# Kernel tuning notes

Measured on AMD Instinct MI355X. Metric: run time of the kernel, lower is better.

The kernel has to match this reference:

```python
import jax, jax.numpy as jnp
import numpy as np

H, C, L = 2, 32, 25
EPS = 1e-5


def setup_inputs() -> dict:
    key = jax.random.key(0)
    ks = jax.random.split(key, 12)
    N, E = 20000, 100000
    x_input = jax.random.normal(ks[0], (N, 5), jnp.float32)
    # edges with no self loops (module uses add_self_loops=True, which first removes them)
    src = jax.random.randint(ks[1], (L, E), 0, N, dtype=jnp.int32)
    off = jax.random.randint(ks[2], (L, E), 1, N, dtype=jnp.int32)
    dst = (src + off) % N
    edge_indices = jnp.stack([src, dst], axis=1)              # [L, 2, E]
    edge_weights = jax.random.uniform(ks[3], (L, E, 1), jnp.float32)
    g = lambda k, shp, fan: jax.random.normal(k, shp, jnp.float32) / np.float32(np.sqrt(fan))
    return {
        "x_input": x_input,
        "edge_indices": edge_indices,
        "edge_weights": edge_weights,
        "Wl": g(ks[4], (L, 5, H * C), 5),
        "bl": jnp.zeros((L, H * C), jnp.float32),
        "Wr": g(ks[5], (L, 5, H * C), 5),
        "br": jnp.zeros((L, H * C), jnp.float32),
        "We": g(ks[6], (L, 1, H * C), 1),
        "att": g(ks[7], (L, H, C), C),
        "conv_bias": jnp.zeros((L, C), jnp.float32),
        "gamma1": jnp.ones((L, C), jnp.float32),
        "beta1": jnp.zeros((L, C), jnp.float32),
        "W1": g(ks[8], (800, 800), 800),
        "b1": jnp.zeros((800,), jnp.float32),
        "W2": g(ks[9], (800, 5), 800),
        "b2": jnp.zeros((5,), jnp.float32),
    }


def reference(x_input, edge_indices, edge_weights, Wl, bl, Wr, br, We, att,
              conv_bias, gamma1, beta1, W1, b1, W2, b2):
    N = x_input.shape[0]
    loops = jnp.arange(N, dtype=edge_indices.dtype)

    def layer(carry, p):
        ei, ew, wl, bl_, wr, br_, we, a, cb, g_, be_ = p
        src, dst = ei[0], ei[1]
        ones_e = jnp.ones((src.shape[0],), x_input.dtype)
        # add_self_loops with fill_value='mean': loop attr = mean of incoming edge attrs
        cnt = jax.ops.segment_sum(ones_e, dst, num_segments=N)
        loop_attr = jax.ops.segment_sum(ew, dst, num_segments=N) / jnp.maximum(cnt, 1.0)[:, None]
        s2 = jnp.concatenate([src, loops])
        d2 = jnp.concatenate([dst, loops])
        ea = jnp.concatenate([ew, loop_attr], axis=0)          # [E+N, 1]
        xl = (x_input @ wl + bl_).reshape(N, H, C)             # source transform
        xr = (x_input @ wr + br_).reshape(N, H, C)             # target transform
        eh = jax.nn.leaky_relu(xl[s2] + xr[d2] + (ea @ we).reshape(-1, H, C), 0.2)
        alpha = jnp.einsum('ehc,hc->eh', eh, a)                # [E+N, H]
        amax = jax.ops.segment_max(alpha, d2, num_segments=N)
        alpha = jnp.exp(alpha - amax[d2])
        alpha = alpha / jax.ops.segment_sum(alpha, d2, num_segments=N)[d2]
        msg = (xl[s2] * alpha[:, :, None]).reshape(-1, H * C)
        deg = jax.ops.segment_sum(jnp.ones((s2.shape[0],), x_input.dtype), d2, num_segments=N)
        out = (jax.ops.segment_sum(msg, d2, num_segments=N) / deg[:, None]).reshape(N, H, C)
        out = out.mean(axis=1) + cb                            # concat=False -> mean over heads, + bias
        mu = out.mean(axis=0)
        var = out.var(axis=0)                                  # BatchNorm1d, training-mode batch stats
        out = g_ * (out - mu) * jax.lax.rsqrt(var + EPS) + be_
        return carry, jax.nn.leaky_relu(out, 0.01)

    _, hs = jax.lax.scan(layer, None,
                         (edge_indices, edge_weights, Wl, bl, Wr, br, We, att,
                          conv_bias, gamma1, beta1))            # [L, N, C]
    h = jnp.transpose(hs, (1, 0, 2)).reshape(N, L * C)          # cat along feature dim
    h = jax.nn.relu(h @ W1 + b1)
    return h @ W2 + b2
```

## Files before the change

### kernel.cpp

```cpp
#include <hip/hip_runtime.h>
#include <hip/hip_bf16.h>

#define N_NODES 20000
#define N_EDGES 100000
#define N_LAYERS 25
#define NPAD 20096
#define EPS_BN 1e-5f
#define LOG2E 1.44269504088896340736f
#define NL_NN (N_LAYERS * N_NODES)
#define TOTAL_E (N_LAYERS * N_EDGES)
#define SCAN_BLKS ((NL_NN + 1023) / 1024)
#define QUARTER_N 5000
#define CNT_BLKS (N_LAYERS * 4)
#define W1T_END (CNT_BLKS + 700)
#define XPAD_END (W1T_END + 157)
#define HPAD_BLKS 75
#define PREP_BLKS (XPAD_END + HPAD_BLKS)
#define EDGE_BLKS ((TOTAL_E + 1023) / 1024)
#define FILL_BLKS (EDGE_BLKS + SCAN_BLKS)
#define NGRP 14
#define NPW 8
#define NPL (N_NODES / NPW)
#define ATTN_WAVES (NL_NN / NPW)
#define ATTN_BLKS (ATTN_WAVES / 4)

typedef short short8 __attribute__((ext_vector_type(8)));
typedef short short4v __attribute__((ext_vector_type(4)));
typedef float floatx4 __attribute__((ext_vector_type(4)));
typedef float float8v __attribute__((ext_vector_type(8)));
typedef int int8v __attribute__((ext_vector_type(8)));
typedef int int2v __attribute__((ext_vector_type(2)));

template <int PAT>
__device__ __forceinline__ float swz(float v) {
  return __int_as_float(__builtin_amdgcn_ds_swizzle(__float_as_int(v), PAT));
}

template <int CTRL>
__device__ __forceinline__ float dpp_add(float v) {
  int r = __builtin_amdgcn_update_dpp(0, __float_as_int(v), CTRL, 0xF, 0xF, true);
  return v + __int_as_float(r);
}

__device__ __forceinline__ float ldbf(const unsigned short* __restrict__ p, int idx) {
  return __uint_as_float((unsigned)p[idx] << 16);
}

__device__ __forceinline__ unsigned short bfbits(float v) {
  return __builtin_bit_cast(unsigned short, (__hip_bfloat16)v);
}

__device__ __forceinline__ void gl_lds16(const short* g, short* l) {
  __builtin_amdgcn_global_load_lds(
      (const __attribute__((address_space(1))) void*)g,
      (__attribute__((address_space(3))) void*)l, 16, 0, 0);
}

__device__ __forceinline__ int8v sload8(const void* p) {
  int8v r;
  asm volatile(
      "s_load_dwordx8 %0, %1, 0x0\n\t"
      "s_waitcnt lgkmcnt(0)"
      : "=s"(r)
      : "s"(p));
  return r;
}

__device__ __forceinline__ void sload_rp(const void* p, int8v& a, int8v& b) {
  asm volatile(
      "s_load_dwordx8 %0, %2, 0x0\n\t"
      "s_load_dwordx8 %1, %2, 0x20\n\t"
      "s_waitcnt lgkmcnt(0)"
      : "=s"(a), "=s"(b)
      : "s"(p));
}

__device__ __forceinline__ void sload_chunk(const void* p, int8v& r0, int8v& r1,
                                            int8v& r2, int8v& r3) {
  asm volatile(
      "s_load_dwordx8 %0, %4, 0x0\n\t"
      "s_load_dwordx8 %1, %4, 0x20\n\t"
      "s_load_dwordx8 %2, %4, 0x40\n\t"
      "s_load_dwordx8 %3, %4, 0x60\n\t"
      "s_waitcnt lgkmcnt(0)"
      : "=s"(r0), "=s"(r1), "=s"(r2), "=s"(r3)
      : "s"(p));
}

__device__ __forceinline__ void red4(float& p0, float& p1, float& p2, float& p3) {
  asm volatile(
      "s_nop 1\n\t"
      "v_add_f32_dpp %0, %0, %0 quad_perm:[1,0,3,2] row_mask:0xf bank_mask:0xf\n\t"
      "v_add_f32_dpp %1, %1, %1 quad_perm:[1,0,3,2] row_mask:0xf bank_mask:0xf\n\t"
      "v_add_f32_dpp %2, %2, %2 quad_perm:[1,0,3,2] row_mask:0xf bank_mask:0xf\n\t"
      "v_add_f32_dpp %3, %3, %3 quad_perm:[1,0,3,2] row_mask:0xf bank_mask:0xf\n\t"
      "v_add_f32_dpp %0, %0, %0 quad_perm:[2,3,0,1] row_mask:0xf bank_mask:0xf\n\t"
      "v_add_f32_dpp %1, %1, %1 quad_perm:[2,3,0,1] row_mask:0xf bank_mask:0xf\n\t"
      "v_add_f32_dpp %2, %2, %2 quad_perm:[2,3,0,1] row_mask:0xf bank_mask:0xf\n\t"
      "v_add_f32_dpp %3, %3, %3 quad_perm:[2,3,0,1] row_mask:0xf bank_mask:0xf\n\t"
      "v_add_f32_dpp %0, %0, %0 row_half_mirror row_mask:0xf bank_mask:0xf\n\t"
      "v_add_f32_dpp %1, %1, %1 row_half_mirror row_mask:0xf bank_mask:0xf\n\t"
      "v_add_f32_dpp %2, %2, %2 row_half_mirror row_mask:0xf bank_mask:0xf\n\t"
      "v_add_f32_dpp %3, %3, %3 row_half_mirror row_mask:0xf bank_mask:0xf\n\t"
      "v_add_f32_dpp %0, %0, %0 row_mirror row_mask:0xf bank_mask:0xf\n\t"
      "v_add_f32_dpp %1, %1, %1 row_mirror row_mask:0xf bank_mask:0xf\n\t"
      "v_add_f32_dpp %2, %2, %2 row_mirror row_mask:0xf bank_mask:0xf\n\t"
      "v_add_f32_dpp %3, %3, %3 row_mirror row_mask:0xf bank_mask:0xf\n\t"
      "s_nop 1"
      : "+v"(p0), "+v"(p1), "+v"(p2), "+v"(p3));
}

__device__ __forceinline__ float red1(float p) {
  asm volatile(
      "s_nop 1\n\t"
      "v_add_f32_dpp %0, %0, %0 quad_perm:[1,0,3,2] row_mask:0xf bank_mask:0xf\n\t"
      "s_nop 1\n\t"
      "v_add_f32_dpp %0, %0, %0 quad_perm:[2,3,0,1] row_mask:0xf bank_mask:0xf\n\t"
      "s_nop 1\n\t"
      "v_add_f32_dpp %0, %0, %0 row_half_mirror row_mask:0xf bank_mask:0xf\n\t"
      "s_nop 1\n\t"
      "v_add_f32_dpp %0, %0, %0 row_mirror row_mask:0xf bank_mask:0xf\n\t"
      "s_nop 1"
      : "+v"(p));
  return p;
}

__global__ __launch_bounds__(1024) void prep_kernel(
    const int* __restrict__ ei, const float* __restrict__ x,
    const float* __restrict__ W1, int* __restrict__ cnt,
    int* __restrict__ rank, float* __restrict__ xpad,
    __hip_bfloat16* __restrict__ W1bT, unsigned short* __restrict__ hn) {
  __shared__ int smem[QUARTER_N];
  int b = blockIdx.x;
  if (b < CNT_BLKS) {
    int l = b >> 2, base = (b & 3) * QUARTER_N;
    for (int i = threadIdx.x; i < QUARTER_N; i += 1024) smem[i] = 0;
    __syncthreads();
    const int* dstp = ei + (size_t)l * 2 * N_EDGES + N_EDGES;
    int* rkp = rank + l * N_EDGES;
    for (int e = threadIdx.x; e < N_EDGES; e += 1024) {
      int d = dstp[e] - base;
      if ((unsigned)d < (unsigned)QUARTER_N) rkp[e] = atomicAdd(&smem[d], 1);
    }
    __syncthreads();
    int* outp = cnt + l * N_NODES + base;
    for (int i = threadIdx.x; i < QUARTER_N; i += 1024) outp[i] = smem[i];
  } else if (b < W1T_END) {
    float* tile = (float*)smem;
    int bb = b - CNT_BLKS;
    int j0 = (bb % 28) * 32, k0 = (bb / 28) * 32;
    int tx = threadIdx.x & 31, ty = threadIdx.x >> 5;
    tile[ty * 33 + tx] = (j0 + tx < 800) ? W1[(k0 + ty) * 800 + j0 + tx] : 0.f;
    __syncthreads();
    W1bT[(size_t)(j0 + ty) * 800 + k0 + tx] = (__hip_bfloat16)tile[tx * 33 + ty];
  } else if (b < XPAD_END) {
    int idx = (b - W1T_END) * 1024 + threadIdx.x;
    if (idx < N_NODES * 8) {
      int nn = idx >> 3, k = idx & 7;
      xpad[idx] = (k < 5) ? x[nn * 5 + k] : 0.f;
    }
  } else {
    int idx = (b - XPAD_END) * 1024 + threadIdx.x;
    const int per_l = (NPAD - N_NODES) * 32;
    if (idx < N_LAYERS * per_l) {
      int l = idx / per_l;
      int rem = idx - l * per_l;
      hn[((size_t)l * NPAD + N_NODES) * 32 + rem] = 0;
    }
  }
}

__global__ __launch_bounds__(1024) void scan_a(const int* __restrict__ cnt,
                                               int* __restrict__ scn,
                                               int* __restrict__ btot,
                                               float* __restrict__ gsum,
                                               float* __restrict__ gsumsq) {
  int t = threadIdx.x, b = blockIdx.x;
  int i = b * 1024 + t;
  int lane = t & 63, wv = t >> 6;
  int v = (i < NL_NN) ? cnt[i] : 0;
  int sc = v;
#pragma unroll
  for (int off = 1; off < 64; off <<= 1) {
    int u = __shfl_up(sc, off);
    if (lane >= off) sc += u;
  }
  __shared__ int ws[16];
  if (lane == 63) ws[wv] = sc;
  __syncthreads();
  if (t < 16) {
    int xx = ws[t];
#pragma unroll
    for (int off = 1; off < 16; off <<= 1) {
      int u = __shfl_up(xx, off);
      if (t >= off) xx += u;
    }
    ws[t] = xx;
  }
  __syncthreads();
  int bofs = wv ? ws[wv - 1] : 0;
  if (i < NL_NN) scn[i] = bofs + sc - v;
  if (t == 0) btot[b] = ws[15];
  if (b == 200 && t < N_LAYERS * 32) {
    gsum[t] = 0.f;
    gsumsq[t] = 0.f;
  }
}

__global__ __launch_bounds__(512) void scan_b(const int* __restrict__ btot,
                                              int* __restrict__ boff) {
  int t = threadIdx.x;
  int lane = t & 63, wv = t >> 6;
  int v = (t < SCAN_BLKS) ? btot[t] : 0;
  int sc = v;
#pragma unroll
  for (int off = 1; off < 64; off <<= 1) {
    int u = __shfl_up(sc, off);
    if (lane >= off) sc += u;
  }
  __shared__ int ws[8];
  if (lane == 63) ws[wv] = sc;
  __syncthreads();
  if (t < 8) {
    int xx = ws[t];
#pragma unroll
    for (int off = 1; off < 8; off <<= 1) {
      int u = __shfl_up(xx, off);
      if (t >= off) xx += u;
    }
    ws[t] = xx;
  }
  __syncthreads();
  int bofs = wv ? ws[wv - 1] : 0;
  if (t < SCAN_BLKS) boff[t] = bofs + sc - v;
}

__global__ __launch_bounds__(1024) void fill_kernel(const int* __restrict__ ei,
                                                    const float* __restrict__ ew,
                                                    const int* __restrict__ scn,
                                                    const int* __restrict__ boff,
                                                    const int* __restrict__ rank,
                                                    const float* __restrict__ xpad,
                                                    int* __restrict__ rowptr,
                                                    float* __restrict__ epf) {
  int b = blockIdx.x;
  if (b < EDGE_BLKS) {
    int idx = b * 1024 + threadIdx.x;
    if (idx >= TOTAL_E) return;
    int l = idx / N_EDGES, e = idx - l * N_EDGES;
    int src = ei[(size_t)l * 2 * N_EDGES + e];
    int dst = ei[(size_t)l * 2 * N_EDGES + N_EDGES + e];
    int g = l * N_NODES + dst;
    int pos = scn[g] + boff[g >> 10] + rank[idx];
    float w = ew[(size_t)l * N_EDGES + e];
    float4 xv = *(const float4*)(xpad + (size_t)src * 8);
    float x4v = xpad[(size_t)src * 8 + 4];
    float8v r;
    r[0] = w; r[1] = xv.x; r[2] = xv.y; r[3] = xv.z; r[4] = xv.w; r[5] = x4v;
    r[6] = 0.f; r[7] = 0.f;
    *(float8v*)(epf + (size_t)pos * 8) = r;
  } else {
    int i = (b - EDGE_BLKS) * 1024 + threadIdx.x;
    if (i < NL_NN) rowptr[i] = scn[i] + boff[i >> 10];
    if (i < 31) rowptr[NL_NN + i] = TOTAL_E;
    if (i < 4) {
      float8v z = {0.f, 0.f, 0.f, 0.f, 0.f, 0.f, 0.f, 0.f};
      *(float8v*)(epf + (size_t)(TOTAL_E + i) * 8) = z;
    }
  }
}

__global__ __launch_bounds__(256) void attn_kernel(
    const float* __restrict__ xpad, const int* __restrict__ rowptr,
    const float* __restrict__ epf,
    const float* __restrict__ Wl, const float* __restrict__ bl,
    const float* __restrict__ Wr, const float* __restrict__ br,
    const float* __restrict__ We, const float* __restrict__ att,
    const float* __restrict__ cbias, unsigned short* __restrict__ out_pre) {
  int b = blockIdx.x;
  const int q = ATTN_BLKS >> 3, r = ATTN_BLKS & 7;
  int xcd = b & 7, ib = b >> 3;
  int nb = (xcd < r ? xcd * (q + 1) : r * (q + 1) + (xcd - r) * q) + ib;
  int wid = __builtin_amdgcn_readfirstlane(nb * 4 + (threadIdx.x >> 6));
  int lane = threadIdx.x & 63;
  int l = wid / NPL;
  int n0 = (wid - l * NPL) * NPW;

  float wlv0 = Wl[(l * 5 + 0) * 64 + lane];
  float wlv1 = Wl[(l * 5 + 1) * 64 + lane];
  float wlv2 = Wl[(l * 5 + 2) * 64 + lane];
  float wlv3 = Wl[(l * 5 + 3) * 64 + lane];
  float wlv4 = Wl[(l * 5 + 4) * 64 + lane];
  float wr0 = Wr[(l * 5 + 0) * 64 + lane];
  float wr1 = Wr[(l * 5 + 1) * 64 + lane];
  float wr2 = Wr[(l * 5 + 2) * 64 + lane];
  float wr3 = Wr[(l * 5 + 3) * 64 + lane];
  float wr4 = Wr[(l * 5 + 4) * 64 + lane];
  float blv = bl[l * 64 + lane];
  float brv = br[l * 64 + lane];
  float wev = We[l * 64 + lane];
  float att2v = att[l * 64 + lane] * LOG2E;
  float cbv = cbias[l * 32 + (lane & 31)];

  int8v rpa, rpb;
  sload_rp(rowptr + (size_t)wid * 8, rpa, rpb);

#pragma unroll
  for (int i = 0; i < NPW; i++) {
    int st = rpa[i & 7];
    int en = (i == 7) ? rpb[0] : rpa[(i + 1) & 7];
    int cnt = en - st;

    int8v xn = sload8(xpad + (size_t)(n0 + i) * 8);
    float x0 = __int_as_float(xn[0]), x1 = __int_as_float(xn[1]);
    float x2 = __int_as_float(xn[2]), x3 = __int_as_float(xn[3]);
    float x4 = __int_as_float(xn[4]);
    float xrn = brv, xln = blv;
    xrn = fmaf(x0, wr0, xrn); xrn = fmaf(x1, wr1, xrn);
    xrn = fmaf(x2, wr2, xrn); xrn = fmaf(x3, wr3, xrn);
    xrn = fmaf(x4, wr4, xrn);
    xln = fmaf(x0, wlv0, xln); xln = fmaf(x1, wlv1, xln);
    xln = fmaf(x2, wlv2, xln); xln = fmaf(x3, wlv3, xln);
    xln = fmaf(x4, wlv4, xln);

    float ssum = 0.f, acc = 0.f, ewsum = 0.f;
    int nchunk = (cnt + 3) >> 2;
    const float* pch = epf + (size_t)st * 8;
    for (int c = 0; c < nchunk; c++) {
      int8v r0, r1, r2, r3;
      sload_chunk(pch, r0, r1, r2, r3);
      pch += 32;
      int m = cnt - c * 4;
      float xa[4], pk[4], wv[4];
#pragma unroll
      for (int k = 0; k < 4; k++) {
        int8v rr = (k == 0) ? r0 : (k == 1) ? r1 : (k == 2) ? r2 : r3;
        bool ok = k < m;
        int wbits = ok ? rr[0] : 0;
        wv[k] = __int_as_float(wbits);
        float a = fmaf(__int_as_float(rr[1]), wlv0, blv);
        a = fmaf(__int_as_float(rr[2]), wlv1, a);
        a = fmaf(__int_as_float(rr[3]), wlv2, a);
        a = fmaf(__int_as_float(rr[4]), wlv3, a);
        a = fmaf(__int_as_float(rr[5]), wlv4, a);
        xa[k] = a;
        float bias = __int_as_float(ok ? 0 : (int)0xff800000);
        float v = a + fmaf(wv[k], wev, xrn);
        float lk = fmaxf(v, 0.2f * v);
        pk[k] = fmaf(lk, att2v, bias);
      }
      red4(pk[0], pk[1], pk[2], pk[3]);
#pragma unroll
      for (int k = 0; k < 4; k++) pk[k] += swz<0x401F>(pk[k]);
#pragma unroll
      for (int k = 0; k < 4; k++) {
        float pe = __builtin_amdgcn_exp2f(pk[k]);
        ssum += pe;
        acc = fmaf(xa[k], pe, acc);
        ewsum += wv[k];
      }
    }
    {
      float w = ewsum * __builtin_amdgcn_rcpf(fmaxf((float)cnt, 1.f));
      float v = xln + fmaf(w, wev, xrn);
      float lk = fmaxf(v, 0.2f * v);
      float p = red1(lk * att2v);
      p += swz<0x401F>(p);
      float pe = __builtin_amdgcn_exp2f(p);
      ssum += pe;
      acc = fmaf(xln, pe, acc);
    }
    float outv = acc * __builtin_amdgcn_rcpf(ssum * (float)(cnt + 1));
    float o2 = outv + __shfl_xor(outv, 32);
    if (lane < 32)
      out_pre[((size_t)wid * NPW + i) * 32 + lane] = bfbits(0.5f * o2 + cbv);
  }
}

__global__ __launch_bounds__(256) void stats_kernel(const unsigned short* __restrict__ out_pre,
                                                    float* __restrict__ gsum,
                                                    float* __restrict__ gsumsq) {
  int l = blockIdx.x >> 4, chunk = blockIdx.x & 15;
  int t = threadIdx.x;
  int c = t & 31, nsub = t >> 5;
  int n0 = chunk * 1250;
  float s1 = 0.f, s2 = 0.f;
  for (int n = n0 + nsub; n < n0 + 1250; n += 8) {
    float v = ldbf(out_pre, (l * N_NODES + n) * 32 + c);
    s1 += v; s2 += v * v;
  }
  __shared__ float l1[256], l2[256];
  l1[t] = s1; l2[t] = s2;
  __syncthreads();
  for (int off = 128; off >= 32; off >>= 1) {
    if (t < off) { l1[t] += l1[t + off]; l2[t] += l2[t + off]; }
    __syncthreads();
  }
  if (t < 32) {
    atomicAdd(&gsum[l * 32 + t], l1[t]);
    atomicAdd(&gsumsq[l * 32 + t], l2[t]);
  }
}

__global__ __launch_bounds__(256) void norm_kernel(const unsigned short* __restrict__ out_pre,
                                                   const float* __restrict__ gsum,
                                                   const float* __restrict__ gsumsq,
                                                   const float* __restrict__ gamma,
                                                   const float* __restrict__ beta,
                                                   unsigned short* __restrict__ hn) {
  int idx = blockIdx.x * 256 + threadIdx.x;
  int l = idx / (N_NODES * 8);
  int rem = idx - l * (N_NODES * 8);
  int n = rem >> 3, q = rem & 7;
  int c0 = q * 4;
  short4v v4 = *(const short4v*)(out_pre + (l * N_NODES + n) * 32 + c0);
  short4v o;
#pragma unroll
  for (int i = 0; i < 4; i++) {
    int c = c0 + i;
    float mu = gsum[l * 32 + c] * (1.f / N_NODES);
    float var = gsumsq[l * 32 + c] * (1.f / N_NODES) - mu * mu;
    float vv = __uint_as_float((unsigned)(unsigned short)v4[i] << 16);
    float v = gamma[l * 32 + c] * (vv - mu) * rsqrtf(var + EPS_BN) + beta[l * 32 + c];
    v = v > 0.f ? v : 0.01f * v;
    o[i] = (short)bfbits(v);
  }
  *(short4v*)(hn + ((size_t)l * NPAD + n) * 32 + c0) = o;
}

__global__ __launch_bounds__(256) void gemm1_kernel(const short* __restrict__ hn,
                                                    const short* __restrict__ W1bT,
                                                    const float* __restrict__ b1,
                                                    const float* __restrict__ W2,
                                                    float* __restrict__ p) {
  __shared__ __align__(16) short As[128 * 32];
  __shared__ __align__(16) short Bs[128 * 32];
  int t = threadIdx.x;
  int n0 = blockIdx.x * 128, m0 = blockIdx.y * 128;
  int wave = t >> 6, lane = t & 63;
  int wr = wave >> 1, wc = wave & 1;
  int mrow = lane & 15, quad = lane >> 4;
  floatx4 acc[4][4];
#pragma unroll
  for (int i = 0; i < 4; i++)
#pragma unroll
    for (int j = 0; j < 4; j++) acc[i][j] = (floatx4){0.f, 0.f, 0.f, 0.f};

  int r0 = t >> 2, s0 = t & 3;
  int r1 = (t + 256) >> 2, s1 = (t + 256) & 3;
  const short* aG0 = hn + (m0 + r0) * 32 + s0 * 8;
  const short* aG1 = hn + (m0 + r1) * 32 + s1 * 8;
  const short* bG0 = W1bT + (n0 + r0) * 800 + s0 * 8;
  const short* bG1 = W1bT + (n0 + r1) * 800 + s1 * 8;
  const int ak = NPAD * 32;
  short* aD0 = As + wave * 512;
  short* aD1 = As + 2048 + wave * 512;
  short* bD0 = Bs + wave * 512;
  short* bD1 = Bs + 2048 + wave * 512;

  for (int kt = 0; kt < 25; kt++) {
    gl_lds16(aG0, aD0);
    gl_lds16(aG1, aD1);
    gl_lds16(bG0, bD0);
    gl_lds16(bG1, bD1);
    aG0 += ak; aG1 += ak; bG0 += 32; bG1 += 32;
    __syncthreads();
    short8 af[4], bfr[4];
#pragma unroll
    for (int i = 0; i < 4; i++)
      af[i] = *(const short8*)(&As[(wr * 64 + i * 16 + mrow) * 32 + quad * 8]);
#pragma unroll
    for (int j = 0; j < 4; j++)
      bfr[j] = *(const short8*)(&Bs[(wc * 64 + j * 16 + mrow) * 32 + quad * 8]);
#pragma unroll
    for (int i = 0; i < 4; i++)
#pragma unroll
      for (int j = 0; j < 4; j++)
        acc[i][j] = __builtin_amdgcn_mfma_f32_16x16x32_bf16(af[i], bfr[j], acc[i][j], 0, 0, 0);
    __syncthreads();
  }

  float w2v[4][5];
  float b1v[4];
#pragma unroll
  for (int j = 0; j < 4; j++) {
    int col = n0 + wc * 64 + j * 16 + mrow;
    bool ok = col < 800;
    b1v[j] = ok ? b1[col] : 0.f;
#pragma unroll
    for (int jj = 0; jj < 5; jj++) w2v[j][jj] = ok ? W2[col * 5 + jj] : 0.f;
  }
  int grp = blockIdx.x * 2 + wc;
#pragma unroll
  for (int i = 0; i < 4; i++) {
#pragma unroll
    for (int r = 0; r < 4; r++) {
      float s[5] = {0.f, 0.f, 0.f, 0.f, 0.f};
#pragma unroll
      for (int j = 0; j < 4; j++) {
        float v = fmaxf(acc[i][j][r] + b1v[j], 0.f);
#pragma unroll
        for (int jj = 0; jj < 5; jj++) s[jj] = fmaf(v, w2v[j][jj], s[jj]);
      }
#pragma unroll
      for (int jj = 0; jj < 5; jj++) {
        s[jj] = dpp_add<0xB1>(s[jj]);
        s[jj] = dpp_add<0x4E>(s[jj]);
        s[jj] = dpp_add<0x141>(s[jj]);
        s[jj] = dpp_add<0x140>(s[jj]);
      }
      int row = m0 + wr * 64 + i * 16 + quad * 4 + r;
      if (mrow == 0) {
#pragma unroll
        for (int jj = 0; jj < 5; jj++)
          p[(row * NGRP + grp) * 5 + jj] = s[jj];
      }
    }
  }
}

__global__ __launch_bounds__(256) void gemm2r_kernel(const float* __restrict__ p,
                                                     const float* __restrict__ b2,
                                                     float* __restrict__ out) {
  int idx = blockIdx.x * 256 + threadIdx.x;
  if (idx >= N_NODES * 5) return;
  int row = idx / 5, jj = idx - row * 5;
  float s = b2[jj];
#pragma unroll
  for (int g = 0; g < NGRP; g++) s += p[(row * NGRP + g) * 5 + jj];
  out[idx] = s;
}

extern "C" void kernel_launch(void* const* d_in, const int* in_sizes, int n_in,
                              void* d_out, int out_size, void* d_ws, size_t ws_size,
                              hipStream_t stream) {
  const float* x    = (const float*)d_in[0];
  const int*   ei   = (const int*)d_in[1];
  const float* ew   = (const float*)d_in[2];
  const float* Wl   = (const float*)d_in[3];
  const float* bl   = (const float*)d_in[4];
  const float* Wr   = (const float*)d_in[5];
  const float* br   = (const float*)d_in[6];
  const float* We   = (const float*)d_in[7];
  const float* att  = (const float*)d_in[8];
  const float* cb   = (const float*)d_in[9];
  const float* gam  = (const float*)d_in[10];
  const float* bet  = (const float*)d_in[11];
  const float* W1   = (const float*)d_in[12];
  const float* b1   = (const float*)d_in[13];
  const float* W2   = (const float*)d_in[14];
  const float* b2   = (const float*)d_in[15];

  char* ws = (char*)d_ws;
  size_t off = 0;
  auto alloc = [&](size_t bytes) {
    void* p = ws + off;
    off = (off + bytes + 255) & ~(size_t)255;
    return p;
  };
  int* cnt     = (int*)alloc((size_t)NL_NN * 4);
  int* scn     = (int*)alloc((size_t)NL_NN * 4);
  int* btot    = (int*)alloc(SCAN_BLKS * 4);
  int* boff    = (int*)alloc(SCAN_BLKS * 4);
  int* rank    = (int*)alloc((size_t)TOTAL_E * 4);
  int* rowptr  = (int*)alloc((size_t)(NL_NN + 32) * 4);
  float* epf   = (float*)alloc((size_t)TOTAL_E * 32 + 128);
  unsigned short* out_pre = (unsigned short*)alloc((size_t)NL_NN * 32 * 2);
  float* gsum   = (float*)alloc(N_LAYERS * 32 * 4);
  float* gsumsq = (float*)alloc(N_LAYERS * 32 * 4);
  float* xpad   = (float*)alloc((size_t)N_NODES * 8 * 4);
  __hip_bfloat16* w1t = (__hip_bfloat16*)alloc((size_t)896 * 800 * 2);
  float* pbuf = (float*)alloc((size_t)NPAD * NGRP * 5 * 4);
  unsigned short* hn = (unsigned short*)alloc((size_t)N_LAYERS * NPAD * 32 * 2);

  prep_kernel<<<PREP_BLKS, 1024, 0, stream>>>(ei, x, W1, cnt, rank, xpad, w1t, hn);
  scan_a<<<SCAN_BLKS, 1024, 0, stream>>>(cnt, scn, btot, gsum, gsumsq);
  scan_b<<<1, 512, 0, stream>>>(btot, boff);
  fill_kernel<<<FILL_BLKS, 1024, 0, stream>>>(ei, ew, scn, boff, rank, xpad,
                                              rowptr, epf);
  attn_kernel<<<ATTN_BLKS, 256, 0, stream>>>(
      xpad, rowptr, epf, Wl, bl, Wr, br, We, att, cb, out_pre);
  stats_kernel<<<N_LAYERS * 16, 256, 0, stream>>>(out_pre, gsum, gsumsq);
  norm_kernel<<<(NL_NN * 8) / 256, 256, 0, stream>>>(
      out_pre, gsum, gsumsq, gam, bet, hn);
  gemm1_kernel<<<dim3(7, 157), 256, 0, stream>>>(
      (const short*)hn, (const short*)w1t, b1, W2, pbuf);
  gemm2r_kernel<<<(N_NODES * 5 + 255) / 256, 256, 0, stream>>>(
      pbuf, b2, (float*)d_out);
}
```

Before: 496.7 us.

## Stage block's edge records into LDS via direct global-to-LDS loads in attn kernel

Each attention block now cooperatively copies the contiguous range of packed edge records for its 32 nodes into a 16 KB shared buffer using global-to-LDS loads. The per-node edge loop then reads from LDS instead of issuing scalar loads to global memory, falling back to global loads when a block's edges exceed the 512-record capacity. The aim is to replace serialized scalar-memory latency with one bulk prefetch. In exchange it adds a block-wide barrier, LDS use that may lower occupancy, and a larger padded edge buffer so the copy can overrun safely.

```diff
diff --git a/kernel.cpp b/kernel.cpp
--- a/kernel.cpp
+++ b/kernel.cpp
@@ -23,6 +23,7 @@
 #define NPL (N_NODES / NPW)
 #define ATTN_WAVES (NL_NN / NPW)
 #define ATTN_BLKS (ATTN_WAVES / 4)
+#define CAP_E 512
 
 typedef short short8 __attribute__((ext_vector_type(8)));
 typedef short short4v __attribute__((ext_vector_type(4)));
@@ -277,12 +278,28 @@
     const float* __restrict__ Wr, const float* __restrict__ br,
     const float* __restrict__ We, const float* __restrict__ att,
     const float* __restrict__ cbias, unsigned short* __restrict__ out_pre) {
+  __shared__ __align__(16) float ldse[CAP_E * 8];
   int b = blockIdx.x;
   const int q = ATTN_BLKS >> 3, r = ATTN_BLKS & 7;
   int xcd = b & 7, ib = b >> 3;
   int nb = (xcd < r ? xcd * (q + 1) : r * (q + 1) + (xcd - r) * q) + ib;
-  int wid = __builtin_amdgcn_readfirstlane(nb * 4 + (threadIdx.x >> 6));
-  int lane = threadIdx.x & 63;
+  int tid = threadIdx.x;
+  int w = tid >> 6, lane = tid & 63;
+  int wid0 = nb * 4;
+  int wid = __builtin_amdgcn_readfirstlane(wid0 + w);
+
+  int bs = __builtin_amdgcn_readfirstlane(rowptr[wid0 * 8]);
+  int be = __builtin_amdgcn_readfirstlane(rowptr[wid0 * 8 + 32]);
+  int want = be - bs + 4;
+  int staged = want < CAP_E ? want : CAP_E;
+  int rounds = (staged * 32 + 4095) >> 12;
+  const char* srcb = (const char*)epf + (size_t)bs * 32;
+  for (int rr2 = 0; rr2 < rounds; rr2++) {
+    int blk16 = (rr2 * 4 + w) * 64;
+    gl_lds16((const short*)(srcb + (size_t)(blk16 + lane) * 16),
+             (short*)((char*)ldse + (size_t)blk16 * 16));
+  }
+
   int l = wid / NPL;
   int n0 = (wid - l * NPL) * NPW;
 
@@ -305,6 +322,8 @@
   int8v rpa, rpb;
   sload_rp(rowptr + (size_t)wid * 8, rpa, rpb);
 
+  __syncthreads();
+
 #pragma unroll
   for (int i = 0; i < NPW; i++) {
     int st = rpa[i & 7];
@@ -325,24 +344,41 @@
 
     float ssum = 0.f, acc = 0.f, ewsum = 0.f;
     int nchunk = (cnt + 3) >> 2;
-    const float* pch = epf + (size_t)st * 8;
     for (int c = 0; c < nchunk; c++) {
-      int8v r0, r1, r2, r3;
-      sload_chunk(pch, r0, r1, r2, r3);
-      pch += 32;
       int m = cnt - c * 4;
+      int g = st + c * 4;
+      float aw[4], av[4][5];
+      if (g - bs + 4 <= staged) {
+        int co = (g - bs) * 32;
+#pragma unroll
+        for (int k = 0; k < 4; k++) {
+          float4 p0 = *(const float4*)((const char*)ldse + (co + k * 32));
+          float4 p1 = *(const float4*)((const char*)ldse + (co + k * 32 + 16));
+          aw[k] = p0.x;
+          av[k][0] = p0.y; av[k][1] = p0.z; av[k][2] = p0.w;
+          av[k][3] = p1.x; av[k][4] = p1.y;
+        }
+      } else {
+        int8v r0, r1, r2, r3;
+        sload_chunk(epf + (size_t)g * 8, r0, r1, r2, r3);
+#pragma unroll
+        for (int k = 0; k < 4; k++) {
+          int8v rrv = (k == 0) ? r0 : (k == 1) ? r1 : (k == 2) ? r2 : r3;
+          aw[k] = __int_as_float(rrv[0]);
+#pragma unroll
+          for (int j = 0; j < 5; j++) av[k][j] = __int_as_float(rrv[1 + j]);
+        }
+      }
       float xa[4], pk[4], wv[4];
 #pragma unroll
       for (int k = 0; k < 4; k++) {
-        int8v rr = (k == 0) ? r0 : (k == 1) ? r1 : (k == 2) ? r2 : r3;
         bool ok = k < m;
-        int wbits = ok ? rr[0] : 0;
-        wv[k] = __int_as_float(wbits);
-        float a = fmaf(__int_as_float(rr[1]), wlv0, blv);
-        a = fmaf(__int_as_float(rr[2]), wlv1, a);
-        a = fmaf(__int_as_float(rr[3]), wlv2, a);
-        a = fmaf(__int_as_float(rr[4]), wlv3, a);
-        a = fmaf(__int_as_float(rr[5]), wlv4, a);
+        wv[k] = ok ? aw[k] : 0.f;
+        float a = fmaf(av[k][0], wlv0, blv);
+        a = fmaf(av[k][1], wlv1, a);
+        a = fmaf(av[k][2], wlv2, a);
+        a = fmaf(av[k][3], wlv3, a);
+        a = fmaf(av[k][4], wlv4, a);
         xa[k] = a;
         float bias = __int_as_float(ok ? 0 : (int)0xff800000);
         float v = a + fmaf(wv[k], wev, xrn);
@@ -361,8 +397,8 @@
       }
     }
     {
-      float w = ewsum * __builtin_amdgcn_rcpf(fmaxf((float)cnt, 1.f));
-      float v = xln + fmaf(w, wev, xrn);
+      float wsl = ewsum * __builtin_amdgcn_rcpf(fmaxf((float)cnt, 1.f));
+      float v = xln + fmaf(wsl, wev, xrn);
       float lk = fmaxf(v, 0.2f * v);
       float p = red1(lk * att2v);
       p += swz<0x401F>(p);
@@ -564,7 +600,7 @@
   int* boff    = (int*)alloc(SCAN_BLKS * 4);
   int* rank    = (int*)alloc((size_t)TOTAL_E * 4);
   int* rowptr  = (int*)alloc((size_t)(NL_NN + 32) * 4);
-  float* epf   = (float*)alloc((size_t)TOTAL_E * 32 + 128);
+  float* epf   = (float*)alloc((size_t)TOTAL_E * 32 + 32768);
   unsigned short* out_pre = (unsigned short*)alloc((size_t)NL_NN * 32 * 2);
   float* gsum   = (float*)alloc(N_LAYERS * 32 * 4);
   float* gsumsq = (float*)alloc(N_LAYERS * 32 * 4);
```

Result: no change. 492.9 us (-0.8%).

## Materialize self-loop slots in CSR and fuse final reduction via atomics

Applied to the files above, without the earlier changes.

The per-destination edge-weight sum is now accumulated during counting, and each node's self-loop (mean weight plus its features) is written as an extra CSR slot. This lets the attention kernel handle the loop in the same chunked loop instead of a separate cross-lane reduction tail. The gemm2 reduction kernel and its partial buffer are removed. The norm kernel initializes the output with b2, and gemm1 atomically adds its partial row sums into the output. This trades one launch and a tail path for extra CSR storage and float atomics whose summation order is nondeterministic.

```diff
diff --git a/kernel.cpp b/kernel.cpp
--- a/kernel.cpp
+++ b/kernel.cpp
@@ -9,6 +9,7 @@
 #define LOG2E 1.44269504088896340736f
 #define NL_NN (N_LAYERS * N_NODES)
 #define TOTAL_E (N_LAYERS * N_EDGES)
+#define TOTAL_SLOTS (TOTAL_E + NL_NN)
 #define SCAN_BLKS ((NL_NN + 1023) / 1024)
 #define QUARTER_N 5000
 #define CNT_BLKS (N_LAYERS * 4)
@@ -18,7 +19,6 @@
 #define PREP_BLKS (XPAD_END + HPAD_BLKS)
 #define EDGE_BLKS ((TOTAL_E + 1023) / 1024)
 #define FILL_BLKS (EDGE_BLKS + SCAN_BLKS)
-#define NGRP 14
 #define NPW 8
 #define NPL (N_NODES / NPW)
 #define ATTN_WAVES (NL_NN / NPW)
@@ -110,41 +110,39 @@
       : "+v"(p0), "+v"(p1), "+v"(p2), "+v"(p3));
 }
 
-__device__ __forceinline__ float red1(float p) {
-  asm volatile(
-      "s_nop 1\n\t"
-      "v_add_f32_dpp %0, %0, %0 quad_perm:[1,0,3,2] row_mask:0xf bank_mask:0xf\n\t"
-      "s_nop 1\n\t"
-      "v_add_f32_dpp %0, %0, %0 quad_perm:[2,3,0,1] row_mask:0xf bank_mask:0xf\n\t"
-      "s_nop 1\n\t"
-      "v_add_f32_dpp %0, %0, %0 row_half_mirror row_mask:0xf bank_mask:0xf\n\t"
-      "s_nop 1\n\t"
-      "v_add_f32_dpp %0, %0, %0 row_mirror row_mask:0xf bank_mask:0xf\n\t"
-      "s_nop 1"
-      : "+v"(p));
-  return p;
-}
-
 __global__ __launch_bounds__(1024) void prep_kernel(
-    const int* __restrict__ ei, const float* __restrict__ x,
-    const float* __restrict__ W1, int* __restrict__ cnt,
-    int* __restrict__ rank, float* __restrict__ xpad,
+    const int* __restrict__ ei, const float* __restrict__ ew,
+    const float* __restrict__ x, const float* __restrict__ W1,
+    int* __restrict__ cnt, int* __restrict__ rank,
+    float* __restrict__ wsumg, float* __restrict__ xpad,
     __hip_bfloat16* __restrict__ W1bT, unsigned short* __restrict__ hn) {
   __shared__ int smem[QUARTER_N];
+  __shared__ float fsm[QUARTER_N];
   int b = blockIdx.x;
   if (b < CNT_BLKS) {
     int l = b >> 2, base = (b & 3) * QUARTER_N;
-    for (int i = threadIdx.x; i < QUARTER_N; i += 1024) smem[i] = 0;
+    for (int i = threadIdx.x; i < QUARTER_N; i += 1024) {
+      smem[i] = 0;
+      fsm[i] = 0.f;
+    }
     __syncthreads();
     const int* dstp = ei + (size_t)l * 2 * N_EDGES + N_EDGES;
+    const float* ewp = ew + (size_t)l * N_EDGES;
     int* rkp = rank + l * N_EDGES;
     for (int e = threadIdx.x; e < N_EDGES; e += 1024) {
       int d = dstp[e] - base;
-      if ((unsigned)d < (unsigned)QUARTER_N) rkp[e] = atomicAdd(&smem[d], 1);
+      if ((unsigned)d < (unsigned)QUARTER_N) {
+        rkp[e] = atomicAdd(&smem[d], 1);
+        atomicAdd(&fsm[d], ewp[e]);
+      }
     }
     __syncthreads();
     int* outp = cnt + l * N_NODES + base;
-    for (int i = threadIdx.x; i < QUARTER_N; i += 1024) outp[i] = smem[i];
+    float* wp = wsumg + l * N_NODES + base;
+    for (int i = threadIdx.x; i < QUARTER_N; i += 1024) {
+      outp[i] = smem[i];
+      wp[i] = fsm[i];
+    }
   } else if (b < W1T_END) {
     float* tile = (float*)smem;
     int bb = b - CNT_BLKS;
@@ -178,7 +176,7 @@
   int t = threadIdx.x, b = blockIdx.x;
   int i = b * 1024 + t;
   int lane = t & 63, wv = t >> 6;
-  int v = (i < NL_NN) ? cnt[i] : 0;
+  int v = (i < NL_NN) ? cnt[i] + 1 : 0;
   int sc = v;
 #pragma unroll
   for (int off = 1; off < 64; off <<= 1) {
@@ -240,6 +238,7 @@
                                                     const int* __restrict__ scn,
                                                     const int* __restrict__ boff,
                                                     const int* __restrict__ rank,
+                                                    const float* __restrict__ wsumg,
                                                     const float* __restrict__ xpad,
                                                     int* __restrict__ rowptr,
                                                     float* __restrict__ epf) {
@@ -261,11 +260,24 @@
     *(float8v*)(epf + (size_t)pos * 8) = r;
   } else {
     int i = (b - EDGE_BLKS) * 1024 + threadIdx.x;
-    if (i < NL_NN) rowptr[i] = scn[i] + boff[i >> 10];
-    if (i < 31) rowptr[NL_NN + i] = TOTAL_E;
+    if (i < NL_NN) {
+      int st = scn[i] + boff[i >> 10];
+      int en = (i + 1 < NL_NN) ? scn[i + 1] + boff[(i + 1) >> 10] : TOTAL_SLOTS;
+      rowptr[i] = st;
+      int cw = en - st - 1;
+      float wm = wsumg[i] * __builtin_amdgcn_rcpf(fmaxf((float)cw, 1.f));
+      int n = i - (i / N_NODES) * N_NODES;
+      float4 xv = *(const float4*)(xpad + (size_t)n * 8);
+      float x4v = xpad[(size_t)n * 8 + 4];
+      float8v r;
+      r[0] = wm; r[1] = xv.x; r[2] = xv.y; r[3] = xv.z; r[4] = xv.w; r[5] = x4v;
+      r[6] = 0.f; r[7] = 0.f;
+      *(float8v*)(epf + (size_t)(en - 1) * 8) = r;
+    }
+    if (i < 31) rowptr[NL_NN + i] = TOTAL_SLOTS;
     if (i < 4) {
       float8v z = {0.f, 0.f, 0.f, 0.f, 0.f, 0.f, 0.f, 0.f};
-      *(float8v*)(epf + (size_t)(TOTAL_E + i) * 8) = z;
+      *(float8v*)(epf + (size_t)(TOTAL_SLOTS + i) * 8) = z;
     }
   }
 }
@@ -309,45 +321,35 @@
   for (int i = 0; i < NPW; i++) {
     int st = rpa[i & 7];
     int en = (i == 7) ? rpb[0] : rpa[(i + 1) & 7];
-    int cnt = en - st;
+    int valid = en - st;
 
     int8v xn = sload8(xpad + (size_t)(n0 + i) * 8);
-    float x0 = __int_as_float(xn[0]), x1 = __int_as_float(xn[1]);
-    float x2 = __int_as_float(xn[2]), x3 = __int_as_float(xn[3]);
-    float x4 = __int_as_float(xn[4]);
-    float xrn = brv, xln = blv;
-    xrn = fmaf(x0, wr0, xrn); xrn = fmaf(x1, wr1, xrn);
-    xrn = fmaf(x2, wr2, xrn); xrn = fmaf(x3, wr3, xrn);
-    xrn = fmaf(x4, wr4, xrn);
-    xln = fmaf(x0, wlv0, xln); xln = fmaf(x1, wlv1, xln);
-    xln = fmaf(x2, wlv2, xln); xln = fmaf(x3, wlv3, xln);
-    xln = fmaf(x4, wlv4, xln);
-
-    float ssum = 0.f, acc = 0.f, ewsum = 0.f;
-    int nchunk = (cnt + 3) >> 2;
-    const float* pch = epf + (size_t)st * 8;
+    float xrn = brv;
+    xrn = fmaf(__int_as_float(xn[0]), wr0, xrn);
+    xrn = fmaf(__int_as_float(xn[1]), wr1, xrn);
+    xrn = fmaf(__int_as_float(xn[2]), wr2, xrn);
+    xrn = fmaf(__int_as_float(xn[3]), wr3, xrn);
+    xrn = fmaf(__int_as_float(xn[4]), wr4, xrn);
+
+    float ssum = 0.f, acc = 0.f;
+    int nchunk = (valid + 3) >> 2;
     for (int c = 0; c < nchunk; c++) {
       int8v r0, r1, r2, r3;
-      sload_chunk(pch, r0, r1, r2, r3);
-      pch += 32;
-      int m = cnt - c * 4;
-      float xa[4], pk[4], wv[4];
+      sload_chunk(epf + (size_t)(st + c * 4) * 8, r0, r1, r2, r3);
+      int m = valid - c * 4;
+      float xa[4], pk[4];
 #pragma unroll
       for (int k = 0; k < 4; k++) {
         int8v rr = (k == 0) ? r0 : (k == 1) ? r1 : (k == 2) ? r2 : r3;
-        bool ok = k < m;
-        int wbits = ok ? rr[0] : 0;
-        wv[k] = __int_as_float(wbits);
         float a = fmaf(__int_as_float(rr[1]), wlv0, blv);
         a = fmaf(__int_as_float(rr[2]), wlv1, a);
         a = fmaf(__int_as_float(rr[3]), wlv2, a);
         a = fmaf(__int_as_float(rr[4]), wlv3, a);
         a = fmaf(__int_as_float(rr[5]), wlv4, a);
         xa[k] = a;
-        float bias = __int_as_float(ok ? 0 : (int)0xff800000);
-        float v = a + fmaf(wv[k], wev, xrn);
+        float v = a + fmaf(__int_as_float(rr[0]), wev, xrn);
         float lk = fmaxf(v, 0.2f * v);
-        pk[k] = fmaf(lk, att2v, bias);
+        pk[k] = lk * att2v;
       }
       red4(pk[0], pk[1], pk[2], pk[3]);
 #pragma unroll
@@ -355,22 +357,12 @@
 #pragma unroll
       for (int k = 0; k < 4; k++) {
         float pe = __builtin_amdgcn_exp2f(pk[k]);
+        pe = (k < m) ? pe : 0.f;
         ssum += pe;
         acc = fmaf(xa[k], pe, acc);
-        ewsum += wv[k];
       }
     }
-    {
-      float w = ewsum * __builtin_amdgcn_rcpf(fmaxf((float)cnt, 1.f));
-      float v = xln + fmaf(w, wev, xrn);
-      float lk = fmaxf(v, 0.2f * v);
-      float p = red1(lk * att2v);
-      p += swz<0x401F>(p);
-      float pe = __builtin_amdgcn_exp2f(p);
-      ssum += pe;
-      acc = fmaf(xln, pe, acc);
-    }
-    float outv = acc * __builtin_amdgcn_rcpf(ssum * (float)(cnt + 1));
+    float outv = acc * __builtin_amdgcn_rcpf(ssum * (float)valid);
     float o2 = outv + __shfl_xor(outv, 32);
     if (lane < 32)
       out_pre[((size_t)wid * NPW + i) * 32 + lane] = bfbits(0.5f * o2 + cbv);
@@ -407,8 +399,11 @@
                                                    const float* __restrict__ gsumsq,
                                                    const float* __restrict__ gamma,
                                                    const float* __restrict__ beta,
+                                                   const float* __restrict__ b2,
+                                                   float* __restrict__ outg,
                                                    unsigned short* __restrict__ hn) {
   int idx = blockIdx.x * 256 + threadIdx.x;
+  if (idx < N_NODES * 5) outg[idx] = b2[idx % 5];
   int l = idx / (N_NODES * 8);
   int rem = idx - l * (N_NODES * 8);
   int n = rem >> 3, q = rem & 7;
@@ -432,7 +427,7 @@
                                                     const short* __restrict__ W1bT,
                                                     const float* __restrict__ b1,
                                                     const float* __restrict__ W2,
-                                                    float* __restrict__ p) {
+                                                    float* __restrict__ outg) {
   __shared__ __align__(16) short As[128 * 32];
   __shared__ __align__(16) short Bs[128 * 32];
   int t = threadIdx.x;
@@ -490,7 +485,6 @@
 #pragma unroll
     for (int jj = 0; jj < 5; jj++) w2v[j][jj] = ok ? W2[col * 5 + jj] : 0.f;
   }
-  int grp = blockIdx.x * 2 + wc;
 #pragma unroll
   for (int i = 0; i < 4; i++) {
 #pragma unroll
@@ -510,25 +504,13 @@
         s[jj] = dpp_add<0x140>(s[jj]);
       }
       int row = m0 + wr * 64 + i * 16 + quad * 4 + r;
-      if (mrow == 0) {
+      if (mrow == 0 && row < N_NODES) {
 #pragma unroll
         for (int jj = 0; jj < 5; jj++)
-          p[(row * NGRP + grp) * 5 + jj] = s[jj];
+          atomicAdd(&outg[row * 5 + jj], s[jj]);
       }
     }
   }
-}
-
-__global__ __launch_bounds__(256) void gemm2r_kernel(const float* __restrict__ p,
-                                                     const float* __restrict__ b2,
-                                                     float* __restrict__ out) {
-  int idx = blockIdx.x * 256 + threadIdx.x;
-  if (idx >= N_NODES * 5) return;
-  int row = idx / 5, jj = idx - row * 5;
-  float s = b2[jj];
-#pragma unroll
-  for (int g = 0; g < NGRP; g++) s += p[(row * NGRP + g) * 5 + jj];
-  out[idx] = s;
 }
 
 extern "C" void kernel_launch(void* const* d_in, const int* in_sizes, int n_in,
@@ -564,27 +546,26 @@
   int* boff    = (int*)alloc(SCAN_BLKS * 4);
   int* rank    = (int*)alloc((size_t)TOTAL_E * 4);
   int* rowptr  = (int*)alloc((size_t)(NL_NN + 32) * 4);
-  float* epf   = (float*)alloc((size_t)TOTAL_E * 32 + 128);
+  float* wsumg = (float*)alloc((size_t)NL_NN * 4);
+  float* epf   = (float*)alloc((size_t)TOTAL_SLOTS * 32 + 256);
   unsigned short* out_pre = (unsigned short*)alloc((size_t)NL_NN * 32 * 2);
   float* gsum   = (float*)alloc(N_LAYERS * 32 * 4);
   float* gsumsq = (float*)alloc(N_LAYERS * 32 * 4);
   float* xpad   = (float*)alloc((size_t)N_NODES * 8 * 4);
   __hip_bfloat16* w1t = (__hip_bfloat16*)alloc((size_t)896 * 800 * 2);
-  float* pbuf = (float*)alloc((size_t)NPAD * NGRP * 5 * 4);
   unsigned short* hn = (unsigned short*)alloc((size_t)N_LAYERS * NPAD * 32 * 2);
 
-  prep_kernel<<<PREP_BLKS, 1024, 0, stream>>>(ei, x, W1, cnt, rank, xpad, w1t, hn);
+  prep_kernel<<<PREP_BLKS, 1024, 0, stream>>>(ei, ew, x, W1, cnt, rank, wsumg,
+                                              xpad, w1t, hn);
   scan_a<<<SCAN_BLKS, 1024, 0, stream>>>(cnt, scn, btot, gsum, gsumsq);
   scan_b<<<1, 512, 0, stream>>>(btot, boff);
-  fill_kernel<<<FILL_BLKS, 1024, 0, stream>>>(ei, ew, scn, boff, rank, xpad,
-                                              rowptr, epf);
+  fill_kernel<<<FILL_BLKS, 1024, 0, stream>>>(ei, ew, scn, boff, rank, wsumg,
+                                              xpad, rowptr, epf);
   attn_kernel<<<ATTN_BLKS, 256, 0, stream>>>(
       xpad, rowptr, epf, Wl, bl, Wr, br, We, att, cb, out_pre);
   stats_kernel<<<N_LAYERS * 16, 256, 0, stream>>>(out_pre, gsum, gsumsq);
   norm_kernel<<<(NL_NN * 8) / 256, 256, 0, stream>>>(
-      out_pre, gsum, gsumsq, gam, bet, hn);
+      out_pre, gsum, gsumsq, gam, bet, b2, (float*)d_out, hn);
   gemm1_kernel<<<dim3(7, 157), 256, 0, stream>>>(
-      (const short*)hn, (const short*)w1t, b1, W2, pbuf);
-  gemm2r_kernel<<<(N_NODES * 5 + 255) / 256, 256, 0, stream>>>(
-      pbuf, b2, (float*)d_out);
-}
+      (const short*)hn, (const short*)w1t, b1, W2, (float*)d_out);
+}
```

After: 602.2 us. 21.2% more time.
